# Performance work log

Measured on AMD Instinct MI355X. Metric: run time of the kernel, lower is better.

## Reference

```python
import jax, jax.numpy as jnp
import numpy as np

N = 100000
NFEAT = 256
DIMS = [NFEAT, 512, 256, 128, 64, 64]  # last is nhid=64


def spmm(edge_w, src, dst, h):
    # sparse adj @ h : out[d] = sum_{e: dst[e]==d} edge_w[e] * h[src[e]]
    return jax.ops.segment_sum(edge_w[:, None] * h[src], dst, num_segments=N)


def setup_inputs() -> dict:
    key = jax.random.key(0)
    ks = jax.random.split(key, 16)
    x = jax.random.normal(ks[0], (N, NFEAT), dtype=jnp.float32)
    E = 3200000
    src = jax.random.randint(ks[1], (E,), 0, N, dtype=jnp.int32)
    dst = jax.random.randint(ks[2], (E,), 0, N, dtype=jnp.int32)
    edge_w = jax.random.uniform(ks[3], (E,), dtype=jnp.float32)
    inp = {"x": x, "src": src, "dst": dst, "edge_w": edge_w}
    for i in range(5):
        fan_in, fan_out = DIMS[i], DIMS[i + 1]
        std = 1.0 / np.sqrt(fan_in)
        inp[f"W{i+1}"] = jax.random.uniform(ks[4 + 2 * i], (fan_in, fan_out), minval=-std, maxval=std, dtype=jnp.float32)
        inp[f"b{i+1}"] = jax.random.uniform(ks[5 + 2 * i], (fan_out,), minval=-std, maxval=std, dtype=jnp.float32)
    return inp


def reference(x, src, dst, edge_w, W1, b1, W2, b2, W3, b3, W4, b4, W5, b5):
    # GraphConvolution: adj @ (x @ W) + b ; relu between layers; dropout is
    # inference-mode (no-op). Final layer has no relu.
    h = x
    for W, b, act in ((W1, b1, True), (W2, b2, True), (W3, b3, True), (W4, b4, True), (W5, b5, False)):
        h = spmm(edge_w, src, dst, h @ W) + b
        if act:
            h = jax.nn.relu(h)
    return h
```

## Files before the change

### kernel.cpp

```cpp
#include <hip/hip_runtime.h>


typedef __attribute__((ext_vector_type(8))) short short8;
typedef __attribute__((ext_vector_type(4))) float f32x4;

__device__ __forceinline__ ushort f2bf(float f) {
    unsigned u = __float_as_uint(f);
    u += 0x7FFFu + ((u >> 16) & 1u);
    return (ushort)(u >> 16);
}
__device__ __forceinline__ float bfl(unsigned u) { return __uint_as_float(u << 16); }
__device__ __forceinline__ float bfh(unsigned u) { return __uint_as_float(u & 0xFFFF0000u); }

#define RANGES 8
#define EPB 16384


__global__ __launch_bounds__(256) void hist_part(const int* __restrict__ dst,
                                                 int* __restrict__ deg,
                                                 int E, int rspan) {
    int range = blockIdx.x & (RANGES - 1);
    int chunk = blockIdx.x / RANGES;
    int lo = range * rspan;
    int base = chunk * EPB;
    int lim = base + EPB < E ? base + EPB : E;
    for (int e = base + (int)threadIdx.x; e < lim; e += 256) {
        int d = dst[e];
        if (d >= lo && d < lo + rspan) atomicAdd(&deg[d], 1);
    }
}

__global__ __launch_bounds__(256) void scatter_part(const int* __restrict__ src,
                                                    const int* __restrict__ dst,
                                                    const float* __restrict__ ew,
                                                    int* pos,
                                                    unsigned* __restrict__ erec,
                                                    int E, int rspan) {
    int range = blockIdx.x & (RANGES - 1);
    int chunk = blockIdx.x / RANGES;
    int lo = range * rspan;
    int base = chunk * EPB;
    int lim = base + EPB < E ? base + EPB : E;
    for (int e = base + (int)threadIdx.x; e < lim; e += 256) {
        int d = dst[e];
        if (d >= lo && d < lo + rspan) {
            int p = atomicAdd(&pos[d], 1);
            float w = ew[e];
            unsigned w15 = (unsigned)(w * 32768.0f + 0.5f);
            if (w15 > 32767u) w15 = 32767u;
            erec[p] = ((unsigned)src[e] << 15) | w15;
        }
    }
}

__global__ __launch_bounds__(256) void scan_p1(const int* __restrict__ deg,
                                               int* __restrict__ sums, int n) {
    int i = blockIdx.x * 256 + threadIdx.x;
    int v = (i < n) ? deg[i] : 0;
    for (int off = 32; off > 0; off >>= 1) v += __shfl_down(v, off, 64);
    __shared__ int ws[4];
    if ((threadIdx.x & 63) == 0) ws[threadIdx.x >> 6] = v;
    __syncthreads();
    if (threadIdx.x == 0) sums[blockIdx.x] = ws[0] + ws[1] + ws[2] + ws[3];
}

__global__ __launch_bounds__(512) void scan_p2(int* __restrict__ sums,
                                               int* __restrict__ rowptr, int n, int nb) {
    __shared__ int sh[512];
    int v = ((int)threadIdx.x < nb) ? sums[threadIdx.x] : 0;
    sh[threadIdx.x] = v;
    __syncthreads();
    for (int off = 1; off < 512; off <<= 1) {
        int t = ((int)threadIdx.x >= off) ? sh[threadIdx.x - off] : 0;
        __syncthreads();
        sh[threadIdx.x] += t;
        __syncthreads();
    }
    if ((int)threadIdx.x < nb) sums[threadIdx.x] = sh[threadIdx.x] - v;
    if (threadIdx.x == 0) rowptr[n] = sh[511];
}

__global__ __launch_bounds__(256) void scan_p3(const int* __restrict__ deg,
                                               const int* __restrict__ sums,
                                               int* __restrict__ rowptr,
                                               int* __restrict__ pos, int n) {
    __shared__ int sh[256];
    int i = blockIdx.x * 256 + threadIdx.x;
    int v = (i < n) ? deg[i] : 0;
    sh[threadIdx.x] = v;
    __syncthreads();
    for (int off = 1; off < 256; off <<= 1) {
        int t = ((int)threadIdx.x >= off) ? sh[threadIdx.x - off] : 0;
        __syncthreads();
        sh[threadIdx.x] += t;
        __syncthreads();
    }
    int excl = sums[blockIdx.x] + sh[threadIdx.x] - v;
    if (i < n) { rowptr[i] = excl; pos[i] = excl; }
}


__global__ __launch_bounds__(256) void convert_x_kernel(const float* __restrict__ in,
                                                        ushort* __restrict__ out, int n4) {
    int i = blockIdx.x * 256 + threadIdx.x;
    if (i >= n4) return;
    float4 v = reinterpret_cast<const float4*>(in)[i];
    uint2 o;
    o.x = ((unsigned)f2bf(v.y) << 16) | (unsigned)f2bf(v.x);
    o.y = ((unsigned)f2bf(v.w) << 16) | (unsigned)f2bf(v.z);
    reinterpret_cast<uint2*>(out)[i] = o;
}

__global__ __launch_bounds__(256) void convert_wt_kernel(const float* __restrict__ W,
                                                         ushort* __restrict__ WT,
                                                         int K, int M) {
    int i = blockIdx.x * 256 + threadIdx.x;
    if (i >= K * M) return;
    int k = i / M, m = i - k * M;
    WT[(size_t)m * K + k] = f2bf(W[i]);
}


#define EDGE_FMA(r, v)                                            \
    {                                                             \
        float w = (float)((r) & 32767u) * (1.0f / 32768.0f);      \
        acc[0] = fmaf(w, bfl((v).x), acc[0]);                     \
        acc[1] = fmaf(w, bfh((v).x), acc[1]);                     \
        acc[2] = fmaf(w, bfl((v).y), acc[2]);                     \
        acc[3] = fmaf(w, bfh((v).y), acc[3]);                     \
        acc[4] = fmaf(w, bfl((v).z), acc[4]);                     \
        acc[5] = fmaf(w, bfh((v).z), acc[5]);                     \
        acc[6] = fmaf(w, bfl((v).w), acc[6]);                     \
        acc[7] = fmaf(w, bfh((v).w), acc[7]);                     \
    }

template <int FAN, bool OUTF32>
__global__ __launch_bounds__(256) void spmm_gather_bf(
        const ushort* __restrict__ T, const int* __restrict__ rowptr,
        const unsigned* __restrict__ erec, const float* __restrict__ bias,
        void* __restrict__ outp, int N, int doRelu) {
    constexpr int LPR = FAN / 8;
    int g = blockIdx.x * 256 + threadIdx.x;
    int row = g / LPR;
    int lane = g - row * LPR;
    if (row >= N) return;
    const int beg = rowptr[row];
    const int end = rowptr[row + 1];
    float acc[8];
#pragma unroll
    for (int j = 0; j < 8; ++j) acc[j] = 0.0f;

    const ushort* Tl = T + lane * 8;
    int p = beg;
    for (; p + 4 <= end; p += 4) {
        unsigned r0 = erec[p], r1 = erec[p + 1], r2 = erec[p + 2], r3 = erec[p + 3];
        uint4 v0 = *reinterpret_cast<const uint4*>(Tl + (size_t)(r0 >> 15) * FAN);
        uint4 v1 = *reinterpret_cast<const uint4*>(Tl + (size_t)(r1 >> 15) * FAN);
        uint4 v2 = *reinterpret_cast<const uint4*>(Tl + (size_t)(r2 >> 15) * FAN);
        uint4 v3 = *reinterpret_cast<const uint4*>(Tl + (size_t)(r3 >> 15) * FAN);
        EDGE_FMA(r0, v0);
        EDGE_FMA(r1, v1);
        EDGE_FMA(r2, v2);
        EDGE_FMA(r3, v3);
    }
    for (; p < end; ++p) {
        unsigned r0 = erec[p];
        uint4 v0 = *reinterpret_cast<const uint4*>(Tl + (size_t)(r0 >> 15) * FAN);
        EDGE_FMA(r0, v0);
    }
    if (bias != nullptr) {
#pragma unroll
        for (int j = 0; j < 8; ++j) acc[j] += bias[lane * 8 + j];
    }
    if (doRelu) {
#pragma unroll
        for (int j = 0; j < 8; ++j) acc[j] = fmaxf(acc[j], 0.0f);
    }
    if (OUTF32) {
        float* o = (float*)outp + (size_t)row * FAN + lane * 8;
        *reinterpret_cast<float4*>(o)     = make_float4(acc[0], acc[1], acc[2], acc[3]);
        *reinterpret_cast<float4*>(o + 4) = make_float4(acc[4], acc[5], acc[6], acc[7]);
    } else {
        uint4 u;
        u.x = ((unsigned)f2bf(acc[1]) << 16) | (unsigned)f2bf(acc[0]);
        u.y = ((unsigned)f2bf(acc[3]) << 16) | (unsigned)f2bf(acc[2]);
        u.z = ((unsigned)f2bf(acc[5]) << 16) | (unsigned)f2bf(acc[4]);
        u.w = ((unsigned)f2bf(acc[7]) << 16) | (unsigned)f2bf(acc[6]);
        *reinterpret_cast<uint4*>((ushort*)outp + (size_t)row * FAN + lane * 8) = u;
    }
}


template <int BN, int WM, int WN>
__global__ __launch_bounds__(256) void gemm_mfma(const ushort* __restrict__ A,
                                                 const ushort* __restrict__ BT,
                                                 const float* __restrict__ bias,
                                                 ushort* __restrict__ C,
                                                 int N, int K, int M, int doBiasRelu) {
    constexpr int BM = 128, BK = 32;
    constexpr int WROWS = BM / WM;
    constexpr int WCOLS = BN / WN;
    constexpr int MR = WROWS / 16;
    constexpr int NR = WCOLS / 16;
    __shared__ ushort As[BM][BK];
    __shared__ ushort Bs[BN][BK];

    const int tid  = threadIdx.x;
    const int wid  = tid >> 6;
    const int lane = tid & 63;
    const int l16  = lane & 15;
    const int lq   = lane >> 4;
    const int wr   = wid / WN;
    const int wc   = wid % WN;
    const long row0 = (long)blockIdx.x * BM;
    const int  col0 = blockIdx.y * BN;

    f32x4 acc[MR][NR] = {};

    for (int k0 = 0; k0 < K; k0 += BK) {
#pragma unroll
        for (int i = 0; i < (BM * BK / 8) / 256; ++i) {
            int t = tid + i * 256;
            int r = t >> 2;
            int c = t & 3;
            uint4 v = *reinterpret_cast<const uint4*>(A + (row0 + r) * K + k0 + c * 8);
            *reinterpret_cast<uint4*>(&As[r][(c ^ (r & 3)) * 8]) = v;
        }
#pragma unroll
        for (int i = 0; i < (BN * BK / 8) / 256; ++i) {
            int t = tid + i * 256;
            int r = t >> 2;
            int c = t & 3;
            uint4 v = *reinterpret_cast<const uint4*>(BT + (size_t)(col0 + r) * K + k0 + c * 8);
            *reinterpret_cast<uint4*>(&Bs[r][(c ^ (r & 3)) * 8]) = v;
        }
        __syncthreads();

        short8 af[MR], bf[NR];
#pragma unroll
        for (int m = 0; m < MR; ++m) {
            int r = wr * WROWS + m * 16 + l16;
            af[m] = *reinterpret_cast<const short8*>(&As[r][(lq ^ (l16 & 3)) * 8]);
        }
#pragma unroll
        for (int n = 0; n < NR; ++n) {
            int r = wc * WCOLS + n * 16 + l16;
            bf[n] = *reinterpret_cast<const short8*>(&Bs[r][(lq ^ (l16 & 3)) * 8]);
        }
#pragma unroll
        for (int m = 0; m < MR; ++m)
#pragma unroll
            for (int n = 0; n < NR; ++n)
                acc[m][n] = __builtin_amdgcn_mfma_f32_16x16x32_bf16(af[m], bf[n], acc[m][n], 0, 0, 0);
        __syncthreads();
    }

#pragma unroll
    for (int m = 0; m < MR; ++m) {
#pragma unroll
        for (int n = 0; n < NR; ++n) {
            int gcol = col0 + wc * WCOLS + n * 16 + l16;
            float bb = doBiasRelu ? bias[gcol] : 0.0f;
#pragma unroll
            for (int r = 0; r < 4; ++r) {
                long grow = row0 + wr * WROWS + m * 16 + lq * 4 + r;
                if (grow < N) {
                    float f = acc[m][n][r] + bb;
                    if (doBiasRelu) f = fmaxf(f, 0.0f);
                    C[grow * M + gcol] = f2bf(f);
                }
            }
        }
    }
}


extern "C" void kernel_launch(void* const* d_in, const int* in_sizes, int n_in,
                              void* d_out, int out_size, void* d_ws, size_t ws_size,
                              hipStream_t stream) {
    const float* x   = (const float*)d_in[0];
    const int*   src = (const int*)d_in[1];
    const int*   dst = (const int*)d_in[2];
    const float* ew  = (const float*)d_in[3];
    const float* W[5]  = {(const float*)d_in[4], (const float*)d_in[6], (const float*)d_in[8],
                          (const float*)d_in[10], (const float*)d_in[12]};
    const float* b[5]  = {(const float*)d_in[5], (const float*)d_in[7], (const float*)d_in[9],
                          (const float*)d_in[11], (const float*)d_in[13]};
    const int Kd[5] = {256, 512, 256, 128, 64};
    const int Md[5] = {512, 256, 128, 64, 64};

    const int N = in_sizes[0] / 256;
    const int E = in_sizes[1];
    const int Npad = ((N + 127) / 128) * 128;
    const int nb = (N + 255) / 256;

    char*  ws  = (char*)d_ws;
    size_t off = 0;
    ushort* buf0 = (ushort*)(ws + off); off += (size_t)Npad * 512 * 2;
    ushort* buf1 = (ushort*)(ws + off); off += (size_t)Npad * 512 * 2;
    ushort* xb   = (ushort*)(ws + off); off += (size_t)Npad * 256 * 2;
    int* rowptr  = (int*)(ws + off);    off += ((size_t)N + 1) * 4;
    int* deg     = (int*)(ws + off);    off += (size_t)N * 4;
    int* pos     = (int*)(ws + off);    off += (size_t)N * 4;
    int* sums    = (int*)(ws + off);    off += 512 * 4;
    off = (off + 15) & ~(size_t)15;
    unsigned* erec = (unsigned*)(ws + off); off += (size_t)E * 4;
    ushort* WT[5];
    for (int i = 0; i < 5; ++i) { WT[i] = (ushort*)(ws + off); off += (size_t)Kd[i] * Md[i] * 2; }
    (void)ws_size; (void)n_in; (void)out_size;

    const int nchunks = (E + EPB - 1) / EPB;
    const int rspan   = (N + RANGES - 1) / RANGES;

    hipMemsetAsync(deg, 0, (size_t)N * 4, stream);
    hist_part<<<RANGES * nchunks, 256, 0, stream>>>(dst, deg, E, rspan);
    scan_p1<<<nb, 256, 0, stream>>>(deg, sums, N);
    scan_p2<<<1, 512, 0, stream>>>(sums, rowptr, N, nb);
    scan_p3<<<nb, 256, 0, stream>>>(deg, sums, rowptr, pos, N);
    scatter_part<<<RANGES * nchunks, 256, 0, stream>>>(src, dst, ew, pos, erec, E, rspan);

    convert_x_kernel<<<((size_t)N * 64 + 255) / 256, 256, 0, stream>>>(x, xb, N * 64);
    for (int i = 0; i < 5; ++i) {
        int n = Kd[i] * Md[i];
        convert_wt_kernel<<<(n + 255) / 256, 256, 0, stream>>>(W[i], WT[i], Kd[i], Md[i]);
    }

    spmm_gather_bf<256, false><<<((size_t)N * 32 + 255) / 256, 256, 0, stream>>>(
        xb, rowptr, erec, nullptr, buf0, N, 0);
    {
        dim3 g(Npad / 128, 512 / 128);
        gemm_mfma<128, 2, 2><<<g, 256, 0, stream>>>(buf0, WT[0], b[0], buf1, N, 256, 512, 1);
    }
    {
        dim3 g(Npad / 128, 256 / 128);
        gemm_mfma<128, 2, 2><<<g, 256, 0, stream>>>(buf1, WT[1], nullptr, buf0, N, 512, 256, 0);
    }
    spmm_gather_bf<256, false><<<((size_t)N * 32 + 255) / 256, 256, 0, stream>>>(
        buf0, rowptr, erec, b[1], buf1, N, 1);
    {
        dim3 g(Npad / 128, 1);
        gemm_mfma<128, 2, 2><<<g, 256, 0, stream>>>(buf1, WT[2], nullptr, buf0, N, 256, 128, 0);
    }
    spmm_gather_bf<128, false><<<((size_t)N * 16 + 255) / 256, 256, 0, stream>>>(
        buf0, rowptr, erec, b[2], buf1, N, 1);
    {
        dim3 g(Npad / 128, 1);
        gemm_mfma<64, 4, 1><<<g, 256, 0, stream>>>(buf1, WT[3], nullptr, buf0, N, 128, 64, 0);
    }
    spmm_gather_bf<64, false><<<((size_t)N * 8 + 255) / 256, 256, 0, stream>>>(
        buf0, rowptr, erec, b[3], buf1, N, 1);
    {
        dim3 g(Npad / 128, 1);
        gemm_mfma<64, 4, 1><<<g, 256, 0, stream>>>(buf1, WT[4], nullptr, buf0, N, 64, 64, 0);
    }
    spmm_gather_bf<64, true><<<((size_t)N * 8 + 255) / 256, 256, 0, stream>>>(
        buf0, rowptr, erec, b[4], (float*)d_out, N, 0);
}
```

Before: 1.255 ms.

## Fuse prologue kernels, deepen gather unroll, use direct-to-LDS loads in GEMM

Merges the degree histogram, x conversion and the five weight transposes into one prologue kernel, cutting launches. The histogram no longer filters edges by destination range, so each edge is read once but atomics are more scattered. The SpMM gather unroll grows from 4 to 8 edges to keep more loads in flight, at the cost of extra registers. The GEMM uses BK=64 with global_load_lds direct-to-LDS copies and an 8-way XOR swizzle, halving K-loop barrier rounds but doubling shared memory per block.

Result: faster. 1.212 ms, median of 2 (-3.5%).

```diff
diff --git a/kernel.cpp b/kernel.cpp
--- a/kernel.cpp
+++ b/kernel.cpp
@@ -12,22 +12,99 @@
 __device__ __forceinline__ float bfl(unsigned u) { return __uint_as_float(u << 16); }
 __device__ __forceinline__ float bfh(unsigned u) { return __uint_as_float(u & 0xFFFF0000u); }
 
+__device__ __forceinline__ void gl_lds16(const void* g, void* l) {
+    __builtin_amdgcn_global_load_lds(
+        (const __attribute__((address_space(1))) unsigned*)g,
+        (__attribute__((address_space(3))) unsigned*)l, 16, 0, 0);
+}
+
 #define RANGES 8
 #define EPB 16384
-
-
-__global__ __launch_bounds__(256) void hist_part(const int* __restrict__ dst,
-                                                 int* __restrict__ deg,
-                                                 int E, int rspan) {
-    int range = blockIdx.x & (RANGES - 1);
-    int chunk = blockIdx.x / RANGES;
-    int lo = range * rspan;
-    int base = chunk * EPB;
-    int lim = base + EPB < E ? base + EPB : E;
-    for (int e = base + (int)threadIdx.x; e < lim; e += 256) {
-        int d = dst[e];
-        if (d >= lo && d < lo + rspan) atomicAdd(&deg[d], 1);
-    }
+#define HB 2048
+
+
+__global__ __launch_bounds__(256) void prologue_kernel(
+        const int* __restrict__ dst, int* __restrict__ deg, int E,
+        const float* __restrict__ x, ushort* __restrict__ xb, int n4,
+        const float* W1, const float* W2, const float* W3, const float* W4, const float* W5,
+        ushort* T1, ushort* T2, ushort* T3, ushort* T4, ushort* T5) {
+    int bid = blockIdx.x;
+    if (bid < HB) {
+        for (int e = bid * 256 + (int)threadIdx.x; e < E; e += HB * 256)
+            atomicAdd(&deg[dst[e]], 1);
+        return;
+    }
+    bid -= HB;
+    int XB = (n4 + 255) / 256;
+    if (bid < XB) {
+        int i = bid * 256 + threadIdx.x;
+        if (i >= n4) return;
+        float4 v = reinterpret_cast<const float4*>(x)[i];
+        uint2 o;
+        o.x = ((unsigned)f2bf(v.y) << 16) | (unsigned)f2bf(v.x);
+        o.y = ((unsigned)f2bf(v.w) << 16) | (unsigned)f2bf(v.z);
+        reinterpret_cast<uint2*>(xb)[i] = o;
+        return;
+    }
+    bid -= XB;
+    int i = bid * 256 + threadIdx.x;
+    const float* W; ushort* T; int K, M, base;
+    if      (i < 131072) { W = W1; T = T1; K = 256; M = 512; base = 0; }
+    else if (i < 262144) { W = W2; T = T2; K = 512; M = 256; base = 131072; }
+    else if (i < 294912) { W = W3; T = T3; K = 256; M = 128; base = 262144; }
+    else if (i < 303104) { W = W4; T = T4; K = 128; M = 64;  base = 294912; }
+    else if (i < 307200) { W = W5; T = T5; K = 64;  M = 64;  base = 303104; }
+    else return;
+    int l = i - base;
+    int k = l / M, m = l - k * M;
+    T[(size_t)m * K + k] = f2bf(W[l]);
+}
+
+
+__global__ __launch_bounds__(256) void scan_p1(const int* __restrict__ deg,
+                                               int* __restrict__ sums, int n) {
+    int i = blockIdx.x * 256 + threadIdx.x;
+    int v = (i < n) ? deg[i] : 0;
+    for (int off = 32; off > 0; off >>= 1) v += __shfl_down(v, off, 64);
+    __shared__ int ws[4];
+    if ((threadIdx.x & 63) == 0) ws[threadIdx.x >> 6] = v;
+    __syncthreads();
+    if (threadIdx.x == 0) sums[blockIdx.x] = ws[0] + ws[1] + ws[2] + ws[3];
+}
+
+__global__ __launch_bounds__(512) void scan_p2(int* __restrict__ sums,
+                                               int* __restrict__ rowptr, int n, int nb) {
+    __shared__ int sh[512];
+    int v = ((int)threadIdx.x < nb) ? sums[threadIdx.x] : 0;
+    sh[threadIdx.x] = v;
+    __syncthreads();
+    for (int off = 1; off < 512; off <<= 1) {
+        int t = ((int)threadIdx.x >= off) ? sh[threadIdx.x - off] : 0;
+        __syncthreads();
+        sh[threadIdx.x] += t;
+        __syncthreads();
+    }
+    if ((int)threadIdx.x < nb) sums[threadIdx.x] = sh[threadIdx.x] - v;
+    if (threadIdx.x == 0) rowptr[n] = sh[511];
+}
+
+__global__ __launch_bounds__(256) void scan_p3(const int* __restrict__ deg,
+                                               const int* __restrict__ sums,
+                                               int* __restrict__ rowptr,
+                                               int* __restrict__ pos, int n) {
+    __shared__ int sh[256];
+    int i = blockIdx.x * 256 + threadIdx.x;
+    int v = (i < n) ? deg[i] : 0;
+    sh[threadIdx.x] = v;
+    __syncthreads();
+    for (int off = 1; off < 256; off <<= 1) {
+        int t = ((int)threadIdx.x >= off) ? sh[threadIdx.x - off] : 0;
+        __syncthreads();
+        sh[threadIdx.x] += t;
+        __syncthreads();
+    }
+    int excl = sums[blockIdx.x] + sh[threadIdx.x] - v;
+    if (i < n) { rowptr[i] = excl; pos[i] = excl; }
 }
 
 __global__ __launch_bounds__(256) void scatter_part(const int* __restrict__ src,
@@ -53,73 +130,6 @@
     }
 }
 
-__global__ __launch_bounds__(256) void scan_p1(const int* __restrict__ deg,
-                                               int* __restrict__ sums, int n) {
-    int i = blockIdx.x * 256 + threadIdx.x;
-    int v = (i < n) ? deg[i] : 0;
-    for (int off = 32; off > 0; off >>= 1) v += __shfl_down(v, off, 64);
-    __shared__ int ws[4];
-    if ((threadIdx.x & 63) == 0) ws[threadIdx.x >> 6] = v;
-    __syncthreads();
-    if (threadIdx.x == 0) sums[blockIdx.x] = ws[0] + ws[1] + ws[2] + ws[3];
-}
-
-__global__ __launch_bounds__(512) void scan_p2(int* __restrict__ sums,
-                                               int* __restrict__ rowptr, int n, int nb) {
-    __shared__ int sh[512];
-    int v = ((int)threadIdx.x < nb) ? sums[threadIdx.x] : 0;
-    sh[threadIdx.x] = v;
-    __syncthreads();
-    for (int off = 1; off < 512; off <<= 1) {
-        int t = ((int)threadIdx.x >= off) ? sh[threadIdx.x - off] : 0;
-        __syncthreads();
-        sh[threadIdx.x] += t;
-        __syncthreads();
-    }
-    if ((int)threadIdx.x < nb) sums[threadIdx.x] = sh[threadIdx.x] - v;
-    if (threadIdx.x == 0) rowptr[n] = sh[511];
-}
-
-__global__ __launch_bounds__(256) void scan_p3(const int* __restrict__ deg,
-                                               const int* __restrict__ sums,
-                                               int* __restrict__ rowptr,
-                                               int* __restrict__ pos, int n) {
-    __shared__ int sh[256];
-    int i = blockIdx.x * 256 + threadIdx.x;
-    int v = (i < n) ? deg[i] : 0;
-    sh[threadIdx.x] = v;
-    __syncthreads();
-    for (int off = 1; off < 256; off <<= 1) {
-        int t = ((int)threadIdx.x >= off) ? sh[threadIdx.x - off] : 0;
-        __syncthreads();
-        sh[threadIdx.x] += t;
-        __syncthreads();
-    }
-    int excl = sums[blockIdx.x] + sh[threadIdx.x] - v;
-    if (i < n) { rowptr[i] = excl; pos[i] = excl; }
-}
-
-
-__global__ __launch_bounds__(256) void convert_x_kernel(const float* __restrict__ in,
-                                                        ushort* __restrict__ out, int n4) {
-    int i = blockIdx.x * 256 + threadIdx.x;
-    if (i >= n4) return;
-    float4 v = reinterpret_cast<const float4*>(in)[i];
-    uint2 o;
-    o.x = ((unsigned)f2bf(v.y) << 16) | (unsigned)f2bf(v.x);
-    o.y = ((unsigned)f2bf(v.w) << 16) | (unsigned)f2bf(v.z);
-    reinterpret_cast<uint2*>(out)[i] = o;
-}
-
-__global__ __launch_bounds__(256) void convert_wt_kernel(const float* __restrict__ W,
-                                                         ushort* __restrict__ WT,
-                                                         int K, int M) {
-    int i = blockIdx.x * 256 + threadIdx.x;
-    if (i >= K * M) return;
-    int k = i / M, m = i - k * M;
-    WT[(size_t)m * K + k] = f2bf(W[i]);
-}
-
 
 #define EDGE_FMA(r, v)                                            \
     {                                                             \
@@ -152,16 +162,16 @@
 
     const ushort* Tl = T + lane * 8;
     int p = beg;
-    for (; p + 4 <= end; p += 4) {
-        unsigned r0 = erec[p], r1 = erec[p + 1], r2 = erec[p + 2], r3 = erec[p + 3];
-        uint4 v0 = *reinterpret_cast<const uint4*>(Tl + (size_t)(r0 >> 15) * FAN);
-        uint4 v1 = *reinterpret_cast<const uint4*>(Tl + (size_t)(r1 >> 15) * FAN);
-        uint4 v2 = *reinterpret_cast<const uint4*>(Tl + (size_t)(r2 >> 15) * FAN);
-        uint4 v3 = *reinterpret_cast<const uint4*>(Tl + (size_t)(r3 >> 15) * FAN);
-        EDGE_FMA(r0, v0);
-        EDGE_FMA(r1, v1);
-        EDGE_FMA(r2, v2);
-        EDGE_FMA(r3, v3);
+    for (; p + 8 <= end; p += 8) {
+        unsigned rr[8];
+        uint4 vv[8];
+#pragma unroll
+        for (int u = 0; u < 8; ++u) rr[u] = erec[p + u];
+#pragma unroll
+        for (int u = 0; u < 8; ++u)
+            vv[u] = *reinterpret_cast<const uint4*>(Tl + (size_t)(rr[u] >> 15) * FAN);
+#pragma unroll
+        for (int u = 0; u < 8; ++u) EDGE_FMA(rr[u], vv[u]);
     }
     for (; p < end; ++p) {
         unsigned r0 = erec[p];
@@ -197,11 +207,13 @@
                                                  const float* __restrict__ bias,
                                                  ushort* __restrict__ C,
                                                  int N, int K, int M, int doBiasRelu) {
-    constexpr int BM = 128, BK = 32;
+    constexpr int BM = 128, BK = 64;
     constexpr int WROWS = BM / WM;
     constexpr int WCOLS = BN / WN;
     constexpr int MR = WROWS / 16;
     constexpr int NR = WCOLS / 16;
+    constexpr int AISS = (BM * BK / 8) / 256;
+    constexpr int BISS = (BN * BK / 8) / 256;
     __shared__ ushort As[BM][BK];
     __shared__ ushort Bs[BN][BK];
 
@@ -219,39 +231,44 @@
 
     for (int k0 = 0; k0 < K; k0 += BK) {
 #pragma unroll
-        for (int i = 0; i < (BM * BK / 8) / 256; ++i) {
-            int t = tid + i * 256;
-            int r = t >> 2;
-            int c = t & 3;
-            uint4 v = *reinterpret_cast<const uint4*>(A + (row0 + r) * K + k0 + c * 8);
-            *reinterpret_cast<uint4*>(&As[r][(c ^ (r & 3)) * 8]) = v;
-        }
-#pragma unroll
-        for (int i = 0; i < (BN * BK / 8) / 256; ++i) {
-            int t = tid + i * 256;
-            int r = t >> 2;
-            int c = t & 3;
-            uint4 v = *reinterpret_cast<const uint4*>(BT + (size_t)(col0 + r) * K + k0 + c * 8);
-            *reinterpret_cast<uint4*>(&Bs[r][(c ^ (r & 3)) * 8]) = v;
-        }
-        __syncthreads();
-
-        short8 af[MR], bf[NR];
-#pragma unroll
-        for (int m = 0; m < MR; ++m) {
-            int r = wr * WROWS + m * 16 + l16;
-            af[m] = *reinterpret_cast<const short8*>(&As[r][(lq ^ (l16 & 3)) * 8]);
-        }
-#pragma unroll
-        for (int n = 0; n < NR; ++n) {
-            int r = wc * WCOLS + n * 16 + l16;
-            bf[n] = *reinterpret_cast<const short8*>(&Bs[r][(lq ^ (l16 & 3)) * 8]);
-        }
-#pragma unroll
-        for (int m = 0; m < MR; ++m)
-#pragma unroll
-            for (int n = 0; n < NR; ++n)
-                acc[m][n] = __builtin_amdgcn_mfma_f32_16x16x32_bf16(af[m], bf[n], acc[m][n], 0, 0, 0);
+        for (int j = 0; j < AISS; ++j) {
+            int t  = (wid * AISS + j) * 64 + lane;
+            int r  = t >> 3;
+            int cw = t & 7;
+            const ushort* g = A + (row0 + r) * K + k0 + ((cw ^ (r & 7)) << 3);
+            gl_lds16(g, (char*)&As[0][0] + (size_t)t * 16);
+        }
+#pragma unroll
+        for (int j = 0; j < BISS; ++j) {
+            int t  = (wid * BISS + j) * 64 + lane;
+            int r  = t >> 3;
+            int cw = t & 7;
+            const ushort* g = BT + (size_t)(col0 + r) * K + k0 + ((cw ^ (r & 7)) << 3);
+            gl_lds16(g, (char*)&Bs[0][0] + (size_t)t * 16);
+        }
+        __syncthreads();
+
+        short8 af[2][MR], bf[2][NR];
+#pragma unroll
+        for (int kk = 0; kk < 2; ++kk) {
+#pragma unroll
+            for (int m = 0; m < MR; ++m) {
+                int r = wr * WROWS + m * 16 + l16;
+                af[kk][m] = *reinterpret_cast<const short8*>(&As[r][((kk * 4 + lq) ^ (r & 7)) * 8]);
+            }
+#pragma unroll
+            for (int n = 0; n < NR; ++n) {
+                int r = wc * WCOLS + n * 16 + l16;
+                bf[kk][n] = *reinterpret_cast<const short8*>(&Bs[r][((kk * 4 + lq) ^ (r & 7)) * 8]);
+            }
+        }
+#pragma unroll
+        for (int kk = 0; kk < 2; ++kk)
+#pragma unroll
+            for (int m = 0; m < MR; ++m)
+#pragma unroll
+                for (int n = 0; n < NR; ++n)
+                    acc[m][n] = __builtin_amdgcn_mfma_f32_16x16x32_bf16(af[kk][m], bf[kk][n], acc[m][n], 0, 0, 0);
         __syncthreads();
     }
 
@@ -311,20 +328,19 @@
 
     const int nchunks = (E + EPB - 1) / EPB;
     const int rspan   = (N + RANGES - 1) / RANGES;
+    const int n4 = N * 64;
+    const int XB = (n4 + 255) / 256;
+    const int WB = (307200 + 255) / 256;
 
     hipMemsetAsync(deg, 0, (size_t)N * 4, stream);
-    hist_part<<<RANGES * nchunks, 256, 0, stream>>>(dst, deg, E, rspan);
+    prologue_kernel<<<HB + XB + WB, 256, 0, stream>>>(
+        dst, deg, E, x, xb, n4,
+        W[0], W[1], W[2], W[3], W[4], WT[0], WT[1], WT[2], WT[3], WT[4]);
     scan_p1<<<nb, 256, 0, stream>>>(deg, sums, N);
     scan_p2<<<1, 512, 0, stream>>>(sums, rowptr, N, nb);
     scan_p3<<<nb, 256, 0, stream>>>(deg, sums, rowptr, pos, N);
     scatter_part<<<RANGES * nchunks, 256, 0, stream>>>(src, dst, ew, pos, erec, E, rspan);
 
-    convert_x_kernel<<<((size_t)N * 64 + 255) / 256, 256, 0, stream>>>(x, xb, N * 64);
-    for (int i = 0; i < 5; ++i) {
-        int n = Kd[i] * Md[i];
-        convert_wt_kernel<<<(n + 255) / 256, 256, 0, stream>>>(W[i], WT[i], Kd[i], Md[i]);
-    }
-
     spmm_gather_bf<256, false><<<((size_t)N * 32 + 255) / 256, 256, 0, stream>>>(
         xb, rowptr, erec, nullptr, buf0, N, 0);
     {
```
